# Kernel optimization log

Hardware: AMD Instinct MI355X
Metric: run time of the kernel (lower is better)

## Reference

```python
import jax, jax.numpy as jnp
import numpy as np

N, E, NG = 50000, 800000, 256          # nodes, edges, graphs
NODE, EDGE, HID, OUT = 64, 16, 64, 1   # feature dims
NUM_LAYERS = 3


def _lin(key, fan_in, fan_out):
    # torch Linear default init: U(-1/sqrt(fan_in), 1/sqrt(fan_in))
    kw, kb = jax.random.split(key)
    bound = 1.0 / np.sqrt(fan_in)
    W = jax.random.uniform(kw, (fan_in, fan_out), jnp.float32, -bound, bound)
    b = jax.random.uniform(kb, (fan_out,), jnp.float32, -bound, bound)
    return W, b


def setup_inputs() -> dict:
    key = jax.random.key(0)
    ks = jax.random.split(key, 8)
    x = jax.random.normal(ks[0], (N, NODE), jnp.float32)
    edge_attr = jax.random.normal(ks[1], (E, EDGE), jnp.float32)
    edge_index = jax.random.randint(ks[2], (2, E), 0, N, dtype=jnp.int32)
    batch = jnp.sort(jax.random.randint(ks[3], (N,), 0, NG, dtype=jnp.int32))
    W_nh, b_nh = _lin(ks[4], NODE, HID)                 # node_to_hidden
    W_mh, b_mh = _lin(ks[5], 2 * HID + EDGE, HID)       # message_to_hidden
    W_om, b_om = _lin(ks[6], 2 * HID + NODE, HID)       # outMsgLin
    W_out, b_out = _lin(ks[7], HID, OUT)                # outLin
    return {"x": x, "edge_attr": edge_attr,
            "W_nh": W_nh, "b_nh": b_nh, "W_mh": W_mh, "b_mh": b_mh,
            "W_om": W_om, "b_om": b_om, "W_out": W_out, "b_out": b_out,
            "edge_index": edge_index, "batch": batch}


def reference(x, edge_attr, W_nh, b_nh, W_mh, b_mh, W_om, b_om, W_out, b_out,
              edge_index, batch):
    # h0 = relu(node_to_hidden(x))
    h0 = jax.nn.relu(x @ W_nh + b_nh)                      # [N, HID]

    # add_self_loops: append N self edges, self-loop edge_attr filled with 1.0
    self_idx = jnp.arange(N, dtype=edge_index.dtype)
    src = jnp.concatenate([edge_index[0], self_idx])       # x_j index (source)
    dst = jnp.concatenate([edge_index[1], self_idx])       # x_i index (target)
    ea = jnp.concatenate([edge_attr,
                          jnp.ones((N, EDGE), edge_attr.dtype)], axis=0)

    # MPN: num_layers of gather-concat -> scatter-add -> linear + h0 -> relu
    h = h0
    for _ in range(NUM_LAYERS):
        msg = jnp.concatenate([h[dst], h[src], ea], axis=1)        # [E+N, 2H+EDGE]
        agg = jax.ops.segment_sum(msg, dst, num_segments=N)        # [N, 2H+EDGE]
        h = jax.nn.relu(agg @ W_mh + b_mh + h0)                    # [N, HID]

    # outMsg: message = concat[h_i, h_j, x_j], aggr add, update identity
    out_msg = jnp.concatenate([h[dst], h[src], x[src]], axis=1)    # [E+N, 2H+NODE]
    agg2 = jax.ops.segment_sum(out_msg, dst, num_segments=N)       # [N, 2H+NODE]

    out = jax.nn.relu(agg2 @ W_om + b_om)                          # [N, HID]
    pooled = jax.ops.segment_sum(out, batch, num_segments=NG)      # [NG, HID]
    return pooled @ W_out + b_out                                  # [NG, OUT]
```

## Files before the change

### kernel.cpp

```cpp
#include <hip/hip_runtime.h>
#include <hip/hip_fp16.h>

#define N_NODES 50000
#define N_EDGES 800000
#define NGRAPH  256
#define FDIM    64
#define EDIM    16
#define NT      (N_NODES / 16)
#define SH      8
#define M8      (N_NODES * SH)
#define NB8     ((M8 + 255) / 256)
#define CH8     ((NB8 + 255) / 256)

#define GRPS       8
#define GRP_BLOCKS 256
#define GRID_CF    (GRPS * GRP_BLOCKS)
#define NPG        ((N_NODES + GRPS - 1) / GRPS)

#define SRC_SHARD(s) ((s) >> 13)

using half8  = __attribute__((ext_vector_type(8))) _Float16;
using float4v = __attribute__((ext_vector_type(4))) float;

__device__ __forceinline__ unsigned hmul2u(unsigned a, __half2 m) {
    __half2 r = __hmul2(__builtin_bit_cast(__half2, a), m);
    return __builtin_bit_cast(unsigned, r);
}
__device__ __forceinline__ unsigned packf2(float a, float b) {
    return __builtin_bit_cast(unsigned, __floats2half2_rn(a, b));
}


__global__ __launch_bounds__(256) void k_count(const int* __restrict__ src,
                                               const int* __restrict__ dst,
                                               int* __restrict__ cnt8) {
    int grp = blockIdx.x & (GRPS - 1);
    int bi  = blockIdx.x >> 3;
    int lo = grp * NPG;
    int hi = lo + NPG; if (hi > N_NODES) hi = N_NODES;
    for (int e = bi * 256 + threadIdx.x; e < N_EDGES; e += GRP_BLOCKS * 256) {
        int d = dst[e];
        if (d >= lo && d < hi) atomicAdd(&cnt8[d * SH + SRC_SHARD(src[e])], 1);
    }
}

__global__ void k_cvt(const float* __restrict__ x, __half* __restrict__ x16,
                      const float* __restrict__ edge_attr, __half* __restrict__ ea16) {
    int t = blockIdx.x * blockDim.x + threadIdx.x;
    int stride = gridDim.x * blockDim.x;
    for (int i = t; i < N_NODES * FDIM; i += stride) x16[i] = __float2half(x[i]);
    for (int i = t; i < N_EDGES * EDIM; i += stride) ea16[i] = __float2half(edge_attr[i]);
}

__global__ void k_blksum(const int* __restrict__ cnt8, int* __restrict__ blksum) {
    __shared__ int red[4];
    int b = blockIdx.x, t = threadIdx.x;
    int idx = b * 256 + t;
    int s = (idx < M8) ? cnt8[idx] : 0;
#pragma unroll
    for (int off = 32; off > 0; off >>= 1) s += __shfl_down(s, off, 64);
    int lane = t & 63, wid = t >> 6;
    if (lane == 0) red[wid] = s;
    __syncthreads();
    if (t == 0) blksum[b] = red[0] + red[1] + red[2] + red[3];
}

__global__ void k_scanblk(const int* __restrict__ blksum, int* __restrict__ boff,
                          int* __restrict__ rowp8) {
    __shared__ int sh[256];
    int t = threadIdx.x;
    int base = t * CH8;
    int v[CH8];
    int s = 0;
#pragma unroll
    for (int i = 0; i < CH8; i++) {
        int idx = base + i;
        v[i] = (idx < NB8) ? blksum[idx] : 0;
        s += v[i];
    }
    sh[t] = s;
    __syncthreads();
    for (int off = 1; off < 256; off <<= 1) {
        int u = (t >= off) ? sh[t - off] : 0;
        __syncthreads();
        sh[t] += u;
        __syncthreads();
    }
    int run = (t == 0) ? 0 : sh[t - 1];
#pragma unroll
    for (int i = 0; i < CH8; i++) {
        int idx = base + i;
        if (idx < NB8) boff[idx] = run;
        run += v[i];
    }
    if (t == 255) rowp8[M8] = sh[255];
}

__global__ void k_rowp(const int* __restrict__ cnt8, const int* __restrict__ boff,
                       int* __restrict__ rowp8, int* __restrict__ cur8) {
    __shared__ int sh[256];
    int b = blockIdx.x, t = threadIdx.x;
    int idx = b * 256 + t;
    int v = (idx < M8) ? cnt8[idx] : 0;
    sh[t] = v;
    __syncthreads();
    for (int off = 1; off < 256; off <<= 1) {
        int u = (t >= off) ? sh[t - off] : 0;
        __syncthreads();
        sh[t] += u;
        __syncthreads();
    }
    if (idx < M8) {
        int excl = sh[t] - v + boff[b];
        rowp8[idx] = excl;
        cur8[idx]  = excl;
    }
}

__global__ void k_degf(const int* __restrict__ rowp8, float* __restrict__ degf) {
    int i = blockIdx.x * blockDim.x + threadIdx.x;
    if (i < N_NODES) degf[i] = (float)(rowp8[(i + 1) * SH] - rowp8[i * SH] + 1);
}

__global__ __launch_bounds__(256) void k_fill(const int* __restrict__ src,
                                              const int* __restrict__ dst,
                                              int* __restrict__ cur8,
                                              int* __restrict__ colsrc,
                                              int* __restrict__ coledge) {
    int grp = blockIdx.x & (GRPS - 1);
    int bi  = blockIdx.x >> 3;
    int lo = grp * NPG;
    int hi = lo + NPG; if (hi > N_NODES) hi = N_NODES;
    for (int e = bi * 256 + threadIdx.x; e < N_EDGES; e += GRP_BLOCKS * 256) {
        int d = dst[e];
        if (d >= lo && d < hi) {
            int s = src[e];
            int pos = atomicAdd(&cur8[d * SH + SRC_SHARD(s)], 1);
            colsrc[pos]  = s;
            coledge[pos] = e;
        }
    }
}

#define SROW 136

__global__ __launch_bounds__(256, 4) void k_gmv(
    const __half* __restrict__ hin16,
    const int* __restrict__ rowp8, const int* __restrict__ colsrc,
    const __half* __restrict__ base16, const float* __restrict__ degf,
    const float* __restrict__ Wmh, __half* __restrict__ hout16) {
    __shared__ __align__(16) _Float16 S[2][16 * SROW];
    int lane = threadIdx.x & 63, wid = threadIdx.x >> 6;
    int tile = wid >> 1, h = wid & 1;
    int t = blockIdx.x * 2 + tile;
    int tb = t * 16;
    int g = lane >> 3;
    int c = lane & 7;
    const uint4* h8 = (const uint4*)hin16;

    if (t < NT) {
        int m = h * 8 + g;
        int node = tb + m;
        int beg = rowp8[node * SH], end = rowp8[(node + 1) * SH];
        float a0 = 0, a1 = 0, a2 = 0, a3 = 0, a4 = 0, a5 = 0, a6 = 0, a7 = 0;
        for (int p = beg; p < end; p += 8) {
            int cidx = p + c; if (cidx > end - 1) cidx = end - 1;
            int vj = colsrc[cidx];
#pragma unroll
            for (int k = 0; k < 8; k++) {
                int j = __shfl(vj, g * 8 + k, 64);
                if (p + k < end) {
                    uint4 v = h8[(size_t)j * 8 + c];
                    float2 f0 = __half22float2(__builtin_bit_cast(__half2, v.x));
                    float2 f1 = __half22float2(__builtin_bit_cast(__half2, v.y));
                    float2 f2 = __half22float2(__builtin_bit_cast(__half2, v.z));
                    float2 f3 = __half22float2(__builtin_bit_cast(__half2, v.w));
                    a0 += f0.x; a1 += f0.y; a2 += f1.x; a3 += f1.y;
                    a4 += f2.x; a5 += f2.y; a6 += f3.x; a7 += f3.y;
                }
            }
        }
        uint4 hv = h8[(size_t)node * 8 + c];
        float dg = degf[node];
        __half dh = __float2half(dg);
        __half2 dh2 = __halves2half2(dh, dh);
        float2 f0 = __half22float2(__builtin_bit_cast(__half2, hv.x));
        float2 f1 = __half22float2(__builtin_bit_cast(__half2, hv.y));
        float2 f2 = __half22float2(__builtin_bit_cast(__half2, hv.z));
        float2 f3 = __half22float2(__builtin_bit_cast(__half2, hv.w));
        uint4 s2, s1;
        s2.x = packf2(a0 + f0.x, a1 + f0.y);
        s2.y = packf2(a2 + f1.x, a3 + f1.y);
        s2.z = packf2(a4 + f2.x, a5 + f2.y);
        s2.w = packf2(a6 + f3.x, a7 + f3.y);
        s1.x = hmul2u(hv.x, dh2); s1.y = hmul2u(hv.y, dh2);
        s1.z = hmul2u(hv.z, dh2); s1.w = hmul2u(hv.w, dh2);
        uint4* Sw = (uint4*)(&S[tile][m * SROW]);
        Sw[c]     = s2;
        Sw[8 + c] = s1;
    }
    __syncthreads();
    if (t >= NT) return;

    int n = lane & 15, quad = lane >> 4;
    half8 bfr[4][2];
#pragma unroll
    for (int kk = 0; kk < 4; kk++)
#pragma unroll
        for (int i = 0; i < 2; i++) {
            int nn = h * 2 + i;
            half8 tmp;
#pragma unroll
            for (int j = 0; j < 8; j++) {
                int kp = kk * 32 + quad * 8 + j;
                int krow = (kp < 64) ? (64 + kp) : (kp - 64);
                tmp[j] = (_Float16)Wmh[krow * FDIM + nn * 16 + n];
            }
            bfr[kk][i] = tmp;
        }
    float4v acc[2];
#pragma unroll
    for (int i = 0; i < 2; i++)
#pragma unroll
        for (int r = 0; r < 4; r++)
            acc[i][r] = __half2float(base16[(size_t)(tb + quad * 4 + r) * FDIM + (h * 2 + i) * 16 + n]);
    const _Float16* Sr = S[tile];
#pragma unroll
    for (int kk = 0; kk < 4; kk++) {
        half8 a = *(const half8*)(Sr + n * SROW + kk * 32 + quad * 8);
#pragma unroll
        for (int i = 0; i < 2; i++)
            acc[i] = __builtin_amdgcn_mfma_f32_16x16x32_f16(a, bfr[kk][i], acc[i], 0, 0, 0);
    }
#pragma unroll
    for (int i = 0; i < 2; i++)
#pragma unroll
        for (int r = 0; r < 4; r++)
            hout16[(size_t)(tb + quad * 4 + r) * FDIM + (h * 2 + i) * 16 + n] =
                __float2half(fmaxf(acc[i][r], 0.f));
}

__global__ __launch_bounds__(256, 4) void k_gout(
    const __half* __restrict__ hin16,
    const int* __restrict__ rowp8, const int* __restrict__ colsrc,
    const __half* __restrict__ obase16, const float* __restrict__ degf,
    const float* __restrict__ Wom, const float* __restrict__ Wout,
    float* __restrict__ sc) {
    __shared__ __align__(16) _Float16 S[2][16 * SROW];
    __shared__ float part[2][2][16];
    int lane = threadIdx.x & 63, wid = threadIdx.x >> 6;
    int tile = wid >> 1, h = wid & 1;
    int t = blockIdx.x * 2 + tile;
    int tb = t * 16;
    int g = lane >> 3;
    int c = lane & 7;
    const uint4* h8 = (const uint4*)hin16;

    if (t < NT) {
        int m = h * 8 + g;
        int node = tb + m;
        int beg = rowp8[node * SH], end = rowp8[(node + 1) * SH];
        float a0 = 0, a1 = 0, a2 = 0, a3 = 0, a4 = 0, a5 = 0, a6 = 0, a7 = 0;
        for (int p = beg; p < end; p += 8) {
            int cidx = p + c; if (cidx > end - 1) cidx = end - 1;
            int vj = colsrc[cidx];
#pragma unroll
            for (int k = 0; k < 8; k++) {
                int j = __shfl(vj, g * 8 + k, 64);
                if (p + k < end) {
                    uint4 v = h8[(size_t)j * 8 + c];
                    float2 f0 = __half22float2(__builtin_bit_cast(__half2, v.x));
                    float2 f1 = __half22float2(__builtin_bit_cast(__half2, v.y));
                    float2 f2 = __half22float2(__builtin_bit_cast(__half2, v.z));
                    float2 f3 = __half22float2(__builtin_bit_cast(__half2, v.w));
                    a0 += f0.x; a1 += f0.y; a2 += f1.x; a3 += f1.y;
                    a4 += f2.x; a5 += f2.y; a6 += f3.x; a7 += f3.y;
                }
            }
        }
        uint4 hv = h8[(size_t)node * 8 + c];
        float dg = degf[node];
        __half dh = __float2half(dg);
        __half2 dh2 = __halves2half2(dh, dh);
        float2 f0 = __half22float2(__builtin_bit_cast(__half2, hv.x));
        float2 f1 = __half22float2(__builtin_bit_cast(__half2, hv.y));
        float2 f2 = __half22float2(__builtin_bit_cast(__half2, hv.z));
        float2 f3 = __half22float2(__builtin_bit_cast(__half2, hv.w));
        uint4 s2, s1;
        s2.x = packf2(a0 + f0.x, a1 + f0.y);
        s2.y = packf2(a2 + f1.x, a3 + f1.y);
        s2.z = packf2(a4 + f2.x, a5 + f2.y);
        s2.w = packf2(a6 + f3.x, a7 + f3.y);
        s1.x = hmul2u(hv.x, dh2); s1.y = hmul2u(hv.y, dh2);
        s1.z = hmul2u(hv.z, dh2); s1.w = hmul2u(hv.w, dh2);
        uint4* Sw = (uint4*)(&S[tile][m * SROW]);
        Sw[c]     = s2;
        Sw[8 + c] = s1;
    }
    __syncthreads();

    int n = lane & 15, quad = lane >> 4;
    if (t < NT) {
        half8 bfr[4][2];
#pragma unroll
        for (int kk = 0; kk < 4; kk++)
#pragma unroll
            for (int i = 0; i < 2; i++) {
                int nn = h * 2 + i;
                half8 tmp;
#pragma unroll
                for (int j = 0; j < 8; j++) {
                    int kp = kk * 32 + quad * 8 + j;
                    int krow = (kp < 64) ? (64 + kp) : (kp - 64);
                    tmp[j] = (_Float16)Wom[krow * FDIM + nn * 16 + n];
                }
                bfr[kk][i] = tmp;
            }
        float wo0 = Wout[(h * 2 + 0) * 16 + n];
        float wo1 = Wout[(h * 2 + 1) * 16 + n];
        float4v acc[2];
#pragma unroll
        for (int i = 0; i < 2; i++)
#pragma unroll
            for (int r = 0; r < 4; r++)
                acc[i][r] = __half2float(obase16[(size_t)(tb + quad * 4 + r) * FDIM + (h * 2 + i) * 16 + n]);
        const _Float16* Sr = S[tile];
#pragma unroll
        for (int kk = 0; kk < 4; kk++) {
            half8 a = *(const half8*)(Sr + n * SROW + kk * 32 + quad * 8);
#pragma unroll
            for (int i = 0; i < 2; i++)
                acc[i] = __builtin_amdgcn_mfma_f32_16x16x32_f16(a, bfr[kk][i], acc[i], 0, 0, 0);
        }
#pragma unroll
        for (int r = 0; r < 4; r++) {
            float s = fmaxf(acc[0][r], 0.f) * wo0 + fmaxf(acc[1][r], 0.f) * wo1;
            s += __shfl_xor(s, 1, 64);
            s += __shfl_xor(s, 2, 64);
            s += __shfl_xor(s, 4, 64);
            s += __shfl_xor(s, 8, 64);
            if (n == 0) part[tile][h][quad * 4 + r] = s;
        }
    }
    __syncthreads();
    if (t < NT && h == 0 && lane < 16)
        sc[tb + lane] = part[tile][0][lane] + part[tile][1][lane];
}

#define SROW2 72
__global__ __launch_bounds__(256, 4) void k_gxob(
    const __half* __restrict__ x16, const __half* __restrict__ ea16,
    const int* __restrict__ rowp8, const int* __restrict__ colsrc,
    const int* __restrict__ coledge,
    const float* __restrict__ Wom, const float* __restrict__ bom,
    __half* __restrict__ obase16, float* __restrict__ ea) {
    __shared__ __align__(16) _Float16 S[2][16 * SROW2];
    int lane = threadIdx.x & 63, wid = threadIdx.x >> 6;
    int tile = wid >> 1, h = wid & 1;
    int t = blockIdx.x * 2 + tile;
    int tb = t * 16;
    int g = lane >> 3;
    int c = lane & 7;
    const uint4* h8 = (const uint4*)x16;
    const unsigned* eap = (const unsigned*)ea16;

    if (t < NT) {
        int m = h * 8 + g;
        int node = tb + m;
        int beg = rowp8[node * SH], end = rowp8[(node + 1) * SH];
        float a0 = 0, a1 = 0, a2 = 0, a3 = 0, a4 = 0, a5 = 0, a6 = 0, a7 = 0;
        float x0 = 0.f, x1 = 0.f;
        for (int p = beg; p < end; p += 8) {
            int cidx = p + c; if (cidx > end - 1) cidx = end - 1;
            int vs = colsrc[cidx];
            int ve = coledge[cidx];
#pragma unroll
            for (int k = 0; k < 8; k++) {
                int j = __shfl(vs, g * 8 + k, 64);
                int e = __shfl(ve, g * 8 + k, 64);
                if (p + k < end) {
                    uint4 v = h8[(size_t)j * 8 + c];
                    unsigned w = eap[(size_t)e * 8 + c];
                    float2 wf = __half22float2(__builtin_bit_cast(__half2, w));
                    float2 f0 = __half22float2(__builtin_bit_cast(__half2, v.x));
                    float2 f1 = __half22float2(__builtin_bit_cast(__half2, v.y));
                    float2 f2 = __half22float2(__builtin_bit_cast(__half2, v.z));
                    float2 f3 = __half22float2(__builtin_bit_cast(__half2, v.w));
                    a0 += f0.x; a1 += f0.y; a2 += f1.x; a3 += f1.y;
                    a4 += f2.x; a5 += f2.y; a6 += f3.x; a7 += f3.y;
                    x0 += wf.x; x1 += wf.y;
                }
            }
        }
        uint4 xv = h8[(size_t)node * 8 + c];
        float2 f0 = __half22float2(__builtin_bit_cast(__half2, xv.x));
        float2 f1 = __half22float2(__builtin_bit_cast(__half2, xv.y));
        float2 f2 = __half22float2(__builtin_bit_cast(__half2, xv.z));
        float2 f3 = __half22float2(__builtin_bit_cast(__half2, xv.w));
        uint4 sA;
        sA.x = packf2(a0 + f0.x, a1 + f0.y);
        sA.y = packf2(a2 + f1.x, a3 + f1.y);
        sA.z = packf2(a4 + f2.x, a5 + f2.y);
        sA.w = packf2(a6 + f3.x, a7 + f3.y);
        ((uint4*)(&S[tile][m * SROW2]))[c] = sA;
        ((float2*)ea)[(size_t)node * 8 + c] = make_float2(x0, x1);
    }
    __syncthreads();
    if (t >= NT) return;

    int n = lane & 15, quad = lane >> 4;
    half8 bfr[2][2];
#pragma unroll
    for (int kk = 0; kk < 2; kk++)
#pragma unroll
        for (int i = 0; i < 2; i++) {
            int nn = h * 2 + i;
            half8 tmp;
#pragma unroll
            for (int j = 0; j < 8; j++) {
                int kp = kk * 32 + quad * 8 + j;
                tmp[j] = (_Float16)Wom[(128 + kp) * FDIM + nn * 16 + n];
            }
            bfr[kk][i] = tmp;
        }
    float4v acc[2];
#pragma unroll
    for (int i = 0; i < 2; i++) {
        float b = bom[(h * 2 + i) * 16 + n];
#pragma unroll
        for (int r = 0; r < 4; r++) acc[i][r] = b;
    }
    const _Float16* Sr = S[tile];
#pragma unroll
    for (int kk = 0; kk < 2; kk++) {
        half8 a = *(const half8*)(Sr + n * SROW2 + kk * 32 + quad * 8);
#pragma unroll
        for (int i = 0; i < 2; i++)
            acc[i] = __builtin_amdgcn_mfma_f32_16x16x32_f16(a, bfr[kk][i], acc[i], 0, 0, 0);
    }
#pragma unroll
    for (int i = 0; i < 2; i++)
#pragma unroll
        for (int r = 0; r < 4; r++)
            obase16[(size_t)(tb + quad * 4 + r) * FDIM + (h * 2 + i) * 16 + n] =
                __float2half(acc[i][r]);
}

__global__ void k_h0base(const float* __restrict__ x, const float* __restrict__ ea,
                         const float* __restrict__ Wnh, const float* __restrict__ bnh,
                         const float* __restrict__ Wmh, const float* __restrict__ bmh,
                         __half* __restrict__ h0out16, __half* __restrict__ base16) {
    __shared__ __align__(16) float sx[4][FDIM];
    __shared__ __align__(16) float sea[4][EDIM];
    int lane = threadIdx.x & 63;
    int wid  = threadIdx.x >> 6;
    float wnh[FDIM], w3[EDIM];
#pragma unroll
    for (int m = 0; m < FDIM; m++) wnh[m] = Wnh[m * FDIM + lane];
    float csum = 0.f;
#pragma unroll
    for (int m = 0; m < EDIM; m++) {
        w3[m] = Wmh[(2 * FDIM + m) * FDIM + lane];
        csum += w3[m];
    }
    float bnhk = bnh[lane], bmhk = bmh[lane];
    int gw = blockIdx.x * 4 + wid;
    int nw = gridDim.x * 4;
    for (int i = gw; i < N_NODES; i += nw) {
        sx[wid][lane] = x[i * FDIM + lane];
        if (lane < EDIM) sea[wid][lane] = ea[i * EDIM + lane];
        float acc0 = bnhk, acc1 = 0.f, acc2 = 0.f, acc3 = 0.f;
        const float4* s4 = (const float4*)sx[wid];
#pragma unroll
        for (int m4 = 0; m4 < FDIM / 4; m4++) {
            float4 v = s4[m4];
            acc0 = fmaf(v.x, wnh[4 * m4 + 0], acc0);
            acc1 = fmaf(v.y, wnh[4 * m4 + 1], acc1);
            acc2 = fmaf(v.z, wnh[4 * m4 + 2], acc2);
            acc3 = fmaf(v.w, wnh[4 * m4 + 3], acc3);
        }
        float h0 = fmaxf((acc0 + acc2) + (acc1 + acc3), 0.f);
        float b0 = h0 + bmhk + csum, b1 = 0.f, b2 = 0.f, b3 = 0.f;
        const float4* e4 = (const float4*)sea[wid];
#pragma unroll
        for (int m4 = 0; m4 < EDIM / 4; m4++) {
            float4 v = e4[m4];
            b0 = fmaf(v.x, w3[4 * m4 + 0], b0);
            b1 = fmaf(v.y, w3[4 * m4 + 1], b1);
            b2 = fmaf(v.z, w3[4 * m4 + 2], b2);
            b3 = fmaf(v.w, w3[4 * m4 + 3], b3);
        }
        h0out16[i * FDIM + lane] = __float2half(h0);
        base16[i * FDIM + lane]  = __float2half((b0 + b2) + (b1 + b3));
    }
}

__global__ void k_pool(const float* __restrict__ sc, const int* __restrict__ batch,
                       const float* __restrict__ b_out, float* __restrict__ out) {
    __shared__ float red[4];
    int g = blockIdx.x, t = threadIdx.x;
    int lo = 0, hi = N_NODES;
    while (lo < hi) { int mid = (lo + hi) >> 1; if (batch[mid] < g) lo = mid + 1; else hi = mid; }
    int lo2 = lo, hi2 = N_NODES;
    while (lo2 < hi2) { int mid = (lo2 + hi2) >> 1; if (batch[mid] < g + 1) lo2 = mid + 1; else hi2 = mid; }
    float s = 0.f;
    for (int i = lo + t; i < lo2; i += 256) s += sc[i];
#pragma unroll
    for (int off = 32; off > 0; off >>= 1) s += __shfl_down(s, off, 64);
    int lane = t & 63, wid = t >> 6;
    if (lane == 0) red[wid] = s;
    __syncthreads();
    if (t == 0) out[g] = red[0] + red[1] + red[2] + red[3] + b_out[0];
}


extern "C" void kernel_launch(void* const* d_in, const int* in_sizes, int n_in,
                              void* d_out, int out_size, void* d_ws, size_t ws_size,
                              hipStream_t stream) {
    const float* x         = (const float*)d_in[0];
    const float* edge_attr = (const float*)d_in[1];
    const float* Wnh       = (const float*)d_in[2];
    const float* bnh       = (const float*)d_in[3];
    const float* Wmh       = (const float*)d_in[4];
    const float* bmh       = (const float*)d_in[5];
    const float* Wom       = (const float*)d_in[6];
    const float* bom       = (const float*)d_in[7];
    const float* Wout      = (const float*)d_in[8];
    const float* bout      = (const float*)d_in[9];
    const int*   eidx      = (const int*)d_in[10];
    const int*   batch     = (const int*)d_in[11];
    const int*   srcI = eidx;
    const int*   dstI = eidx + N_EDGES;
    float* out = (float*)d_out;
    (void)in_sizes; (void)n_in; (void)out_size;

    char* w = (char*)d_ws;
    size_t off = 0;
    auto take = [&](size_t b) -> void* {
        void* p = w + off;
        off = (off + b + 255) & ~(size_t)255;
        return p;
    };
    float*  ea     = (float*)take((size_t)N_NODES * EDIM * 4);
    int*    cnt8   = (int*)take((size_t)M8 * 4);
    int*    rowp8  = (int*)take((size_t)(M8 + 1) * 4);
    int*    cur8   = (int*)take((size_t)M8 * 4);
    float*  degf   = (float*)take((size_t)N_NODES * 4);
    int*    colsrc = (int*)take((size_t)N_EDGES * 4);
    int*    coledge= (int*)take((size_t)N_EDGES * 4);
    __half* ea16   = (__half*)take((size_t)N_EDGES * EDIM * 2);
    float*  sc     = (float*)take((size_t)N_NODES * 4);
    int*    blks   = (int*)take((size_t)NB8 * 4);
    int*    boff   = (int*)take((size_t)NB8 * 4);
    __half* x16    = (__half*)take((size_t)N_NODES * FDIM * 2);
    __half* hA16   = (__half*)take((size_t)N_NODES * FDIM * 2);
    __half* hB16   = (__half*)take((size_t)N_NODES * FDIM * 2);
    __half* base16 = (__half*)take((size_t)N_NODES * FDIM * 2);
    __half* obase16= (__half*)take((size_t)N_NODES * FDIM * 2);
    (void)ws_size;

    const int G2 = (NT + 1) / 2;

    hipMemsetAsync(cnt8, 0, (size_t)M8 * 4, stream);
    k_count<<<GRID_CF, 256, 0, stream>>>(srcI, dstI, cnt8);
    k_cvt<<<2048, 256, 0, stream>>>(x, x16, edge_attr, ea16);
    k_blksum<<<NB8, 256, 0, stream>>>(cnt8, blks);
    k_scanblk<<<1, 256, 0, stream>>>(blks, boff, rowp8);
    k_rowp<<<NB8, 256, 0, stream>>>(cnt8, boff, rowp8, cur8);
    k_degf<<<(N_NODES + 255) / 256, 256, 0, stream>>>(rowp8, degf);
    k_fill<<<GRID_CF, 256, 0, stream>>>(srcI, dstI, cur8, colsrc, coledge);

    k_gxob<<<G2, 256, 0, stream>>>(x16, ea16, rowp8, colsrc, coledge,
                                   Wom, bom, obase16, ea);
    k_h0base<<<2048, 256, 0, stream>>>(x, ea, Wnh, bnh, Wmh, bmh, hA16, base16);

    k_gmv<<<G2, 256, 0, stream>>>(hA16, rowp8, colsrc, base16, degf, Wmh, hB16);
    k_gmv<<<G2, 256, 0, stream>>>(hB16, rowp8, colsrc, base16, degf, Wmh, hA16);
    k_gmv<<<G2, 256, 0, stream>>>(hA16, rowp8, colsrc, base16, degf, Wmh, hB16);

    k_gout<<<G2, 256, 0, stream>>>(hB16, rowp8, colsrc, obase16, degf, Wom, Wout, sc);
    k_pool<<<NGRAPH, 256, 0, stream>>>(sc, batch, bout, out);
}
```

Measured before the change: 340.0 us.

## Vectorize fp16 conversion, fold degree into rowp, raise gather-kernel occupancy

Rewrites the fp32-to-fp16 conversion kernel to read float4 pairs and write packed 16-byte halves. Removes the separate degree kernel by computing node degree from the shared-memory scan inside k_rowp, which saves one launch. Raises launch_bounds occupancy from 4 to 8 on the three gather/MFMA kernels. Weight fragments are now loaded inside the MFMA loop instead of being preloaded into registers, which lowers register pressure but puts weight loads on the MFMA critical path.

```diff
diff --git a/kernel.cpp b/kernel.cpp
--- a/kernel.cpp
+++ b/kernel.cpp
@@ -48,8 +48,24 @@
                       const float* __restrict__ edge_attr, __half* __restrict__ ea16) {
     int t = blockIdx.x * blockDim.x + threadIdx.x;
     int stride = gridDim.x * blockDim.x;
-    for (int i = t; i < N_NODES * FDIM; i += stride) x16[i] = __float2half(x[i]);
-    for (int i = t; i < N_EDGES * EDIM; i += stride) ea16[i] = __float2half(edge_attr[i]);
+    const float4* x4 = (const float4*)x;
+    uint4* xo = (uint4*)x16;
+    for (int i = t; i < N_NODES * FDIM / 8; i += stride) {
+        float4 a = x4[i * 2], b = x4[i * 2 + 1];
+        uint4 o;
+        o.x = packf2(a.x, a.y); o.y = packf2(a.z, a.w);
+        o.z = packf2(b.x, b.y); o.w = packf2(b.z, b.w);
+        xo[i] = o;
+    }
+    const float4* e4 = (const float4*)edge_attr;
+    uint4* eo = (uint4*)ea16;
+    for (int i = t; i < N_EDGES * EDIM / 8; i += stride) {
+        float4 a = e4[i * 2], b = e4[i * 2 + 1];
+        uint4 o;
+        o.x = packf2(a.x, a.y); o.y = packf2(a.z, a.w);
+        o.z = packf2(b.x, b.y); o.w = packf2(b.z, b.w);
+        eo[i] = o;
+    }
 }
 
 __global__ void k_blksum(const int* __restrict__ cnt8, int* __restrict__ blksum) {
@@ -97,7 +113,8 @@
 }
 
 __global__ void k_rowp(const int* __restrict__ cnt8, const int* __restrict__ boff,
-                       int* __restrict__ rowp8, int* __restrict__ cur8) {
+                       int* __restrict__ rowp8, int* __restrict__ cur8,
+                       float* __restrict__ degf) {
     __shared__ int sh[256];
     int b = blockIdx.x, t = threadIdx.x;
     int idx = b * 256 + t;
@@ -114,12 +131,11 @@
         int excl = sh[t] - v + boff[b];
         rowp8[idx] = excl;
         cur8[idx]  = excl;
-    }
-}
-
-__global__ void k_degf(const int* __restrict__ rowp8, float* __restrict__ degf) {
-    int i = blockIdx.x * blockDim.x + threadIdx.x;
-    if (i < N_NODES) degf[i] = (float)(rowp8[(i + 1) * SH] - rowp8[i * SH] + 1);
+        if ((t & 7) == 7) {
+            int start = (t >= 8) ? sh[t - 8] : 0;
+            degf[b * 32 + (t >> 3)] = (float)(sh[t] - start + 1);
+        }
+    }
 }
 
 __global__ __launch_bounds__(256) void k_fill(const int* __restrict__ src,
@@ -144,7 +160,7 @@
 
 #define SROW 136
 
-__global__ __launch_bounds__(256, 4) void k_gmv(
+__global__ __launch_bounds__(256, 8) void k_gmv(
     const __half* __restrict__ hin16,
     const int* __restrict__ rowp8, const int* __restrict__ colsrc,
     const __half* __restrict__ base16, const float* __restrict__ degf,
@@ -203,34 +219,28 @@
     if (t >= NT) return;
 
     int n = lane & 15, quad = lane >> 4;
-    half8 bfr[4][2];
-#pragma unroll
-    for (int kk = 0; kk < 4; kk++)
+    float4v acc[2];
+#pragma unroll
+    for (int i = 0; i < 2; i++)
+#pragma unroll
+        for (int r = 0; r < 4; r++)
+            acc[i][r] = __half2float(base16[(size_t)(tb + quad * 4 + r) * FDIM + (h * 2 + i) * 16 + n]);
+    const _Float16* Sr = S[tile];
+#pragma unroll
+    for (int kk = 0; kk < 4; kk++) {
+        half8 a = *(const half8*)(Sr + n * SROW + kk * 32 + quad * 8);
 #pragma unroll
         for (int i = 0; i < 2; i++) {
             int nn = h * 2 + i;
-            half8 tmp;
+            half8 w;
 #pragma unroll
             for (int j = 0; j < 8; j++) {
                 int kp = kk * 32 + quad * 8 + j;
                 int krow = (kp < 64) ? (64 + kp) : (kp - 64);
-                tmp[j] = (_Float16)Wmh[krow * FDIM + nn * 16 + n];
+                w[j] = (_Float16)Wmh[krow * FDIM + nn * 16 + n];
             }
-            bfr[kk][i] = tmp;
-        }
-    float4v acc[2];
-#pragma unroll
-    for (int i = 0; i < 2; i++)
-#pragma unroll
-        for (int r = 0; r < 4; r++)
-            acc[i][r] = __half2float(base16[(size_t)(tb + quad * 4 + r) * FDIM + (h * 2 + i) * 16 + n]);
-    const _Float16* Sr = S[tile];
-#pragma unroll
-    for (int kk = 0; kk < 4; kk++) {
-        half8 a = *(const half8*)(Sr + n * SROW + kk * 32 + quad * 8);
-#pragma unroll
-        for (int i = 0; i < 2; i++)
-            acc[i] = __builtin_amdgcn_mfma_f32_16x16x32_f16(a, bfr[kk][i], acc[i], 0, 0, 0);
+            acc[i] = __builtin_amdgcn_mfma_f32_16x16x32_f16(a, w, acc[i], 0, 0, 0);
+        }
     }
 #pragma unroll
     for (int i = 0; i < 2; i++)
@@ -240,7 +250,7 @@
                 __float2half(fmaxf(acc[i][r], 0.f));
 }
 
-__global__ __launch_bounds__(256, 4) void k_gout(
+__global__ __launch_bounds__(256, 8) void k_gout(
     const __half* __restrict__ hin16,
     const int* __restrict__ rowp8, const int* __restrict__ colsrc,
     const __half* __restrict__ obase16, const float* __restrict__ degf,
@@ -301,36 +311,30 @@
 
     int n = lane & 15, quad = lane >> 4;
     if (t < NT) {
-        half8 bfr[4][2];
-#pragma unroll
-        for (int kk = 0; kk < 4; kk++)
+        float wo0 = Wout[(h * 2 + 0) * 16 + n];
+        float wo1 = Wout[(h * 2 + 1) * 16 + n];
+        float4v acc[2];
+#pragma unroll
+        for (int i = 0; i < 2; i++)
+#pragma unroll
+            for (int r = 0; r < 4; r++)
+                acc[i][r] = __half2float(obase16[(size_t)(tb + quad * 4 + r) * FDIM + (h * 2 + i) * 16 + n]);
+        const _Float16* Sr = S[tile];
+#pragma unroll
+        for (int kk = 0; kk < 4; kk++) {
+            half8 a = *(const half8*)(Sr + n * SROW + kk * 32 + quad * 8);
 #pragma unroll
             for (int i = 0; i < 2; i++) {
                 int nn = h * 2 + i;
-                half8 tmp;
+                half8 w;
 #pragma unroll
                 for (int j = 0; j < 8; j++) {
                     int kp = kk * 32 + quad * 8 + j;
                     int krow = (kp < 64) ? (64 + kp) : (kp - 64);
-                    tmp[j] = (_Float16)Wom[krow * FDIM + nn * 16 + n];
+                    w[j] = (_Float16)Wom[krow * FDIM + nn * 16 + n];
                 }
-                bfr[kk][i] = tmp;
+                acc[i] = __builtin_amdgcn_mfma_f32_16x16x32_f16(a, w, acc[i], 0, 0, 0);
             }
-        float wo0 = Wout[(h * 2 + 0) * 16 + n];
-        float wo1 = Wout[(h * 2 + 1) * 16 + n];
-        float4v acc[2];
-#pragma unroll
-        for (int i = 0; i < 2; i++)
-#pragma unroll
-            for (int r = 0; r < 4; r++)
-                acc[i][r] = __half2float(obase16[(size_t)(tb + quad * 4 + r) * FDIM + (h * 2 + i) * 16 + n]);
-        const _Float16* Sr = S[tile];
-#pragma unroll
-        for (int kk = 0; kk < 4; kk++) {
-            half8 a = *(const half8*)(Sr + n * SROW + kk * 32 + quad * 8);
-#pragma unroll
-            for (int i = 0; i < 2; i++)
-                acc[i] = __builtin_amdgcn_mfma_f32_16x16x32_f16(a, bfr[kk][i], acc[i], 0, 0, 0);
         }
 #pragma unroll
         for (int r = 0; r < 4; r++) {
@@ -348,7 +352,7 @@
 }
 
 #define SROW2 72
-__global__ __launch_bounds__(256, 4) void k_gxob(
+__global__ __launch_bounds__(256, 8) void k_gxob(
     const __half* __restrict__ x16, const __half* __restrict__ ea16,
     const int* __restrict__ rowp8, const int* __restrict__ colsrc,
     const int* __restrict__ coledge,
@@ -409,34 +413,28 @@
     if (t >= NT) return;
 
     int n = lane & 15, quad = lane >> 4;
-    half8 bfr[2][2];
-#pragma unroll
-    for (int kk = 0; kk < 2; kk++)
+    float4v acc[2];
+#pragma unroll
+    for (int i = 0; i < 2; i++) {
+        float b = bom[(h * 2 + i) * 16 + n];
+#pragma unroll
+        for (int r = 0; r < 4; r++) acc[i][r] = b;
+    }
+    const _Float16* Sr = S[tile];
+#pragma unroll
+    for (int kk = 0; kk < 2; kk++) {
+        half8 a = *(const half8*)(Sr + n * SROW2 + kk * 32 + quad * 8);
 #pragma unroll
         for (int i = 0; i < 2; i++) {
             int nn = h * 2 + i;
-            half8 tmp;
+            half8 w;
 #pragma unroll
             for (int j = 0; j < 8; j++) {
                 int kp = kk * 32 + quad * 8 + j;
-                tmp[j] = (_Float16)Wom[(128 + kp) * FDIM + nn * 16 + n];
+                w[j] = (_Float16)Wom[(128 + kp) * FDIM + nn * 16 + n];
             }
-            bfr[kk][i] = tmp;
-        }
-    float4v acc[2];
-#pragma unroll
-    for (int i = 0; i < 2; i++) {
-        float b = bom[(h * 2 + i) * 16 + n];
-#pragma unroll
-        for (int r = 0; r < 4; r++) acc[i][r] = b;
-    }
-    const _Float16* Sr = S[tile];
-#pragma unroll
-    for (int kk = 0; kk < 2; kk++) {
-        half8 a = *(const half8*)(Sr + n * SROW2 + kk * 32 + quad * 8);
-#pragma unroll
-        for (int i = 0; i < 2; i++)
-            acc[i] = __builtin_amdgcn_mfma_f32_16x16x32_f16(a, bfr[kk][i], acc[i], 0, 0, 0);
+            acc[i] = __builtin_amdgcn_mfma_f32_16x16x32_f16(a, w, acc[i], 0, 0, 0);
+        }
     }
 #pragma unroll
     for (int i = 0; i < 2; i++)
@@ -566,8 +564,7 @@
     k_cvt<<<2048, 256, 0, stream>>>(x, x16, edge_attr, ea16);
     k_blksum<<<NB8, 256, 0, stream>>>(cnt8, blks);
     k_scanblk<<<1, 256, 0, stream>>>(blks, boff, rowp8);
-    k_rowp<<<NB8, 256, 0, stream>>>(cnt8, boff, rowp8, cur8);
-    k_degf<<<(N_NODES + 255) / 256, 256, 0, stream>>>(rowp8, degf);
+    k_rowp<<<NB8, 256, 0, stream>>>(cnt8, boff, rowp8, cur8, degf);
     k_fill<<<GRID_CF, 256, 0, stream>>>(srcI, dstI, cur8, colsrc, coledge);
 
     k_gxob<<<G2, 256, 0, stream>>>(x16, ea16, rowp8, colsrc, coledge,
```

New measurement: 344.7 us. No clear change (+1.4%).
